# Optimization experiments

Measured on AMD Instinct MI355X. Metric: run time of the kernel, lower is better.

## Reference

```python
import jax, jax.numpy as jnp
import numpy as np

HEADS = 4
DIM_HEAD = 32


def setup_inputs() -> dict:
    key = jax.random.key(0)
    k1, k2, k3, k4, k5 = jax.random.split(key, 5)
    dim = 128
    hidden = HEADS * DIM_HEAD  # 128
    h = w = 384
    x = jax.random.normal(k1, (1, dim, h, w), dtype=jnp.float32)
    # 1x1 conv weights (eqx Conv2d layout: [out_c, in_c, 1, 1]) + biases
    w_qkv = jax.random.normal(k2, (3 * hidden, dim, 1, 1), dtype=jnp.float32) * (1.0 / np.sqrt(dim))
    b_qkv = jax.random.normal(k3, (3 * hidden,), dtype=jnp.float32) * 0.01
    w_out = jax.random.normal(k4, (dim, hidden, 1, 1), dtype=jnp.float32) * (1.0 / np.sqrt(hidden))
    b_out = jax.random.normal(k5, (dim,), dtype=jnp.float32) * 0.01
    return {"x": x, "w_qkv": w_qkv, "b_qkv": b_qkv, "w_out": w_out, "b_out": b_out}


def reference(x, w_qkv, b_qkv, w_out, b_out):
    b, c, h, w = x.shape  # b == 1 (module squeezes batch)
    xs = x[0]  # (c, h, w)
    # 1x1 conv == channel matmul
    qkv = jnp.einsum('oc,chw->ohw', w_qkv[:, :, 0, 0], xs) + b_qkv[:, None, None]
    # rearrange '(qkv heads c) h w -> qkv heads c (h w)'
    qkv = qkv.reshape(3, HEADS, DIM_HEAD, h * w)
    q, k, v = qkv[0], qkv[1], qkv[2]  # each (heads, d, n)
    k = jax.nn.softmax(k, axis=-1)
    # context: (heads, d, e) -- small per-head outer product accumulated over n
    context = jnp.einsum('hdn,hen->hde', k, v)
    out = jnp.einsum('hde,hdn->hen', context, q)  # (heads, e, n)
    out = out.reshape(HEADS * DIM_HEAD, h, w)
    y = jnp.einsum('oc,chw->ohw', w_out[:, :, 0, 0], out) + b_out[:, None, None]
    return y  # (dim, h, w) -- module returns squeezed output
```

## Files before the change

kernel.cpp:

```cpp
#include <hip/hip_runtime.h>
#include <hip/hip_bf16.h>
#include <stdint.h>


#define NPOS 147456
#define NTILES 2304
#define NB1 512

typedef __attribute__((ext_vector_type(8))) short short8;
typedef __attribute__((ext_vector_type(4))) float floatx4;

__device__ __forceinline__ uint16_t f2bf(float f) {
    uint32_t u = __float_as_uint(f);
    return (uint16_t)((u + 0x7fffu + ((u >> 16) & 1u)) >> 16);
}
__device__ __forceinline__ uint32_t pack2(float a, float b) {
#if __has_builtin(__builtin_amdgcn_cvt_pk_bf16_f32)
    auto r = __builtin_amdgcn_cvt_pk_bf16_f32(a, b);
    uint32_t u; __builtin_memcpy(&u, &r, sizeof(u));
    return u;
#else
    return (uint32_t)f2bf(a) | ((uint32_t)f2bf(b) << 16);
#endif
}

#define XS_STRIDE 68
#define PS_STRIDE 36

__global__ __launch_bounds__(256, 2) void k1_ctx(
    const float* __restrict__ x, const float* __restrict__ w_qkv,
    const float* __restrict__ b_qkv, float* __restrict__ cpart, int nb1)
{
    __shared__ uint32_t Xs[2][64 * XS_STRIDE];
    __shared__ uint32_t Ps[256 * PS_STRIDE];

    const int t = threadIdx.x;
    const int lane = t & 63;
    const int wavu = __builtin_amdgcn_readfirstlane(t >> 6);
    const int m = lane & 15, quad = lane >> 4;
    const int kvbase = wavu * 64;
    const bool is_k = (wavu < 2);
    const int c0 = wavu * 32;

    short8 wfr[4][4];
    float biasv[4];
    #pragma unroll
    for (int kt = 0; kt < 4; ++kt) {
        const int row = 128 + kvbase + kt * 16 + m;
        biasv[kt] = b_qkv[row];
        #pragma unroll
        for (int ks = 0; ks < 4; ++ks) {
            const float* p = w_qkv + row * 128 + ks * 32 + quad * 8;
            short8 w;
            #pragma unroll
            for (int j = 0; j < 8; ++j) w[j] = (short)f2bf(p[j]);
            wfr[kt][ks] = w;
        }
    }

    floatx4 acc2[4];
    #pragma unroll
    for (int i = 0; i < 4; ++i) acc2[i] = (floatx4){0.f, 0.f, 0.f, 0.f};
    float sacc[4] = {0.f, 0.f, 0.f, 0.f};

    {
        const int nofs = blockIdx.x * 64 + lane;
        float pf[32];
        #pragma unroll
        for (int i = 0; i < 32; ++i)
            pf[i] = x[(c0 + i) * NPOS + nofs];
        #pragma unroll
        for (int i = 0; i < 8; ++i) {
            uint2 w;
            w.x = pack2(pf[i * 4 + 0], pf[i * 4 + 1]);
            w.y = pack2(pf[i * 4 + 2], pf[i * 4 + 3]);
            *(uint2*)&Xs[0][lane * XS_STRIDE + (c0 + i * 4) / 2] = w;
        }
    }
    __syncthreads();

    int cur = 0;
    for (int tile = blockIdx.x; tile < NTILES; tile += nb1) {
        const int tn = tile + nb1;
        float pf[32];
        if (tn < NTILES) {
            const int nofs = tn * 64 + lane;
            #pragma unroll
            for (int i = 0; i < 32; ++i)
                pf[i] = x[(c0 + i) * NPOS + nofs];
        }
        #pragma unroll
        for (int nt = 0; nt < 4; ++nt) {
            short8 afr[4];
            #pragma unroll
            for (int ks = 0; ks < 4; ++ks)
                afr[ks] = *(const short8*)&Xs[cur][(nt * 16 + m) * XS_STRIDE + ks * 16 + quad * 4];
            floatx4 pa[4];
            #pragma unroll
            for (int kt = 0; kt < 4; ++kt) pa[kt] = (floatx4){0.f, 0.f, 0.f, 0.f};
            #pragma unroll
            for (int ks = 0; ks < 4; ++ks)
                #pragma unroll
                for (int kt = 0; kt < 4; ++kt)
                    pa[kt] = __builtin_amdgcn_mfma_f32_16x16x32_bf16(afr[ks], wfr[kt][ks], pa[kt], 0, 0, 0);
            #pragma unroll
            for (int kt = 0; kt < 4; ++kt) {
                float v0 = pa[kt][0] + biasv[kt];
                float v1 = pa[kt][1] + biasv[kt];
                float v2 = pa[kt][2] + biasv[kt];
                float v3 = pa[kt][3] + biasv[kt];
                if (is_k) {
                    v0 = __expf(v0); v1 = __expf(v1);
                    v2 = __expf(v2); v3 = __expf(v3);
                    sacc[kt] += (v0 + v1) + (v2 + v3);
                }
                uint2 w;
                w.x = pack2(v0, v1);
                w.y = pack2(v2, v3);
                const int kvrow = kvbase + kt * 16 + m;
                *(uint2*)&Ps[kvrow * PS_STRIDE + nt * 8 + quad * 2] = w;
            }
        }
        __syncthreads();
        #pragma unroll
        for (int ks = 0; ks < 2; ++ks) {
            short8 ea[2], vb[2];
            #pragma unroll
            for (int dt = 0; dt < 2; ++dt)
                ea[dt] = *(const short8*)&Ps[(wavu * 32 + dt * 16 + m) * PS_STRIDE + ks * 16 + quad * 4];
            #pragma unroll
            for (int et = 0; et < 2; ++et)
                vb[et] = *(const short8*)&Ps[(128 + wavu * 32 + et * 16 + m) * PS_STRIDE + ks * 16 + quad * 4];
            #pragma unroll
            for (int dt = 0; dt < 2; ++dt)
                #pragma unroll
                for (int et = 0; et < 2; ++et)
                    acc2[dt * 2 + et] = __builtin_amdgcn_mfma_f32_16x16x32_bf16(ea[dt], vb[et], acc2[dt * 2 + et], 0, 0, 0);
        }
        if (tn < NTILES) {
            #pragma unroll
            for (int i = 0; i < 8; ++i) {
                uint2 w;
                w.x = pack2(pf[i * 4 + 0], pf[i * 4 + 1]);
                w.y = pack2(pf[i * 4 + 2], pf[i * 4 + 3]);
                *(uint2*)&Xs[cur ^ 1][lane * XS_STRIDE + (c0 + i * 4) / 2] = w;
            }
        }
        __syncthreads();
        cur ^= 1;
    }
    float* __restrict__ dst = cpart + (size_t)blockIdx.x * 4224;
    #pragma unroll
    for (int dt = 0; dt < 2; ++dt)
        #pragma unroll
        for (int et = 0; et < 2; ++et)
            #pragma unroll
            for (int r = 0; r < 4; ++r) {
                const int d = dt * 16 + quad * 4 + r, e = et * 16 + m;
                dst[wavu * 1024 + d * 32 + e] = acc2[dt * 2 + et][r];
            }
    if (is_k) {
        #pragma unroll
        for (int kt = 0; kt < 4; ++kt) {
            float s = sacc[kt];
            s += __shfl_down(s, 32, 64);
            s += __shfl_down(s, 16, 64);
            if (lane < 16) dst[4096 + kvbase + kt * 16 + lane] = s;
        }
    }
}

__global__ void k2a(const float* __restrict__ cpart, float* __restrict__ ctxP, int nb1)
{
    const int u = blockIdx.x * 256 + threadIdx.x;
    if (u >= 4224 * 8) return;
    const int j = u % 4224, p = u / 4224;
    float s = 0.f;
    for (int b = p; b < nb1; b += 8) s += cpart[(size_t)b * 4224 + j];
    ctxP[p * 4224 + j] = s;
}

__global__ __launch_bounds__(128) void k2bc(
    const float* __restrict__ ctxP, const float* __restrict__ w_out,
    const float* __restrict__ w_qkv, const float* __restrict__ b_qkv,
    const float* __restrict__ b_out, float* __restrict__ Bm, float* __restrict__ cvec)
{
    __shared__ float ctx33[128 * 33];
    __shared__ float Ss[128];
    __shared__ float Arow[128];
    __shared__ float red[128];
    const int o = blockIdx.x, t = threadIdx.x;
    for (int j = t; j < 4224; j += 128) {
        float s = 0.f;
        #pragma unroll
        for (int p = 0; p < 8; ++p) s += ctxP[p * 4224 + j];
        if (j < 4096) ctx33[(j >> 5) * 33 + (j & 31)] = s;
        else          Ss[j - 4096] = s;
    }
    __syncthreads();
    {
        const int h = t >> 5;
        float s = 0.f;
        #pragma unroll
        for (int e = 0; e < 32; ++e)
            s = fmaf(w_out[o * 128 + h * 32 + e], ctx33[t * 33 + e], s);
        Arow[t] = s / Ss[t];
    }
    __syncthreads();
    {
        float s = 0.f;
        #pragma unroll 16
        for (int hd = 0; hd < 128; ++hd)
            s = fmaf(Arow[hd], w_qkv[hd * 128 + t], s);
        Bm[o * 128 + t] = s;
    }
    red[t] = Arow[t] * b_qkv[t];
    __syncthreads();
    if (t == 0) {
        float cs = b_out[o];
        #pragma unroll 8
        for (int i = 0; i < 128; ++i) cs += red[i];
        cvec[o] = cs;
    }
}

__global__ __launch_bounds__(256) void k3(
    const float* __restrict__ x, const float* __restrict__ Bm,
    const float* __restrict__ cvec, float* __restrict__ y)
{
    __shared__ uint32_t Xs[64 * XS_STRIDE];
    const int t = threadIdx.x, lane = t & 63;
    const int wavu = __builtin_amdgcn_readfirstlane(t >> 6);
    const int m = lane & 15, quad = lane >> 4;
    const int n0 = blockIdx.x * 64;
    const int c0 = wavu * 32;

    short8 bfr[2][4];
    float cv[2];
    #pragma unroll
    for (int ot = 0; ot < 2; ++ot) {
        const int o = (wavu * 2 + ot) * 16 + m;
        cv[ot] = cvec[o];
        #pragma unroll
        for (int ks = 0; ks < 4; ++ks) {
            const float* p = Bm + o * 128 + ks * 32 + quad * 8;
            short8 w;
            #pragma unroll
            for (int j = 0; j < 8; ++j) w[j] = (short)f2bf(p[j]);
            bfr[ot][ks] = w;
        }
    }
    {
        const int nofs = n0 + lane;
        float pf[32];
        #pragma unroll
        for (int i = 0; i < 32; ++i)
            pf[i] = x[(c0 + i) * NPOS + nofs];
        #pragma unroll
        for (int i = 0; i < 8; ++i) {
            uint2 w;
            w.x = pack2(pf[i * 4 + 0], pf[i * 4 + 1]);
            w.y = pack2(pf[i * 4 + 2], pf[i * 4 + 3]);
            *(uint2*)&Xs[lane * XS_STRIDE + (c0 + i * 4) / 2] = w;
        }
    }
    __syncthreads();
    floatx4 acc[2][4];
    #pragma unroll
    for (int ot = 0; ot < 2; ++ot)
        #pragma unroll
        for (int nt = 0; nt < 4; ++nt) acc[ot][nt] = (floatx4){0.f, 0.f, 0.f, 0.f};
    #pragma unroll
    for (int nt = 0; nt < 4; ++nt) {
        short8 afr[4];
        #pragma unroll
        for (int ks = 0; ks < 4; ++ks)
            afr[ks] = *(const short8*)&Xs[(nt * 16 + m) * XS_STRIDE + ks * 16 + quad * 4];
        #pragma unroll
        for (int ks = 0; ks < 4; ++ks)
            #pragma unroll
            for (int ot = 0; ot < 2; ++ot)
                acc[ot][nt] = __builtin_amdgcn_mfma_f32_16x16x32_bf16(afr[ks], bfr[ot][ks], acc[ot][nt], 0, 0, 0);
    }
    #pragma unroll
    for (int ot = 0; ot < 2; ++ot) {
        const int o = (wavu * 2 + ot) * 16 + m;
        #pragma unroll
        for (int nt = 0; nt < 4; ++nt) {
            floatx4 v = acc[ot][nt];
            v.x += cv[ot]; v.y += cv[ot]; v.z += cv[ot]; v.w += cv[ot];
            *(floatx4*)(y + (size_t)o * NPOS + n0 + nt * 16 + quad * 4) = v;
        }
    }
}

extern "C" void kernel_launch(void* const* d_in, const int* in_sizes, int n_in,
                              void* d_out, int out_size, void* d_ws, size_t ws_size,
                              hipStream_t stream)
{
    const float* x     = (const float*)d_in[0];
    const float* w_qkv = (const float*)d_in[1];
    const float* b_qkv = (const float*)d_in[2];
    const float* w_out = (const float*)d_in[3];
    const float* b_out = (const float*)d_in[4];
    float* y = (float*)d_out;

    const size_t tail = (size_t)(8 * 4224 + 16384 + 128) * 4;
    int nb1 = NB1;
    if (ws_size < tail + (size_t)nb1 * 16896) {
        long cap = ((long)ws_size - (long)tail) / 16896;
        nb1 = (int)cap;
        if (nb1 < 1) nb1 = 1;
        if (nb1 > NB1) nb1 = NB1;
    }
    char* wsb = (char*)d_ws;
    float* cpart = (float*)wsb;
    float* ctxP  = (float*)(wsb + (size_t)nb1 * 16896);
    float* Bm    = ctxP + 8 * 4224;
    float* cvec  = Bm + 16384;

    hipLaunchKernelGGL(k1_ctx, dim3(nb1), dim3(256), 0, stream, x, w_qkv, b_qkv, cpart, nb1);
    hipLaunchKernelGGL(k2a, dim3(132), dim3(256), 0, stream, cpart, ctxP, nb1);
    hipLaunchKernelGGL(k2bc, dim3(128), dim3(128), 0, stream, ctxP, w_out, w_qkv, b_qkv, b_out, Bm, cvec);
    hipLaunchKernelGGL(k3, dim3(NTILES), dim3(256), 0, stream, x, Bm, cvec, y);
}
```

Baseline: 206.2 us.

## Give each wave its own head's K/V, deepen prefetch, pre-pack Bm to bf16

In the context kernel, each wave now computes both K and V projections for its own head and writes them to a private LDS slice. This removes the cross-wave barrier between the projection and the context MFMA stages. The loop is unrolled by two with two register prefetch buffers, so global loads of x run two tiles ahead, at the cost of more registers. The combined output matrix is written as packed bf16 by k2bc, so k3 loads ready MFMA fragments instead of converting floats, and k3 issues its x loads before the weight loads.

Result: no change. 203.8 us (-1.2%).

```diff
diff --git a/kernel.cpp b/kernel.cpp
--- a/kernel.cpp
+++ b/kernel.cpp
@@ -27,6 +27,72 @@
 #define XS_STRIDE 68
 #define PS_STRIDE 36
 
+__device__ __forceinline__ void k1_load(const float* __restrict__ xb, float* pf) {
+    #pragma unroll
+    for (int i = 0; i < 32; ++i) pf[i] = xb[(size_t)i * NPOS];
+}
+__device__ __forceinline__ void k1_store(uint32_t* Xsbuf, const float* pf, int lane, int c0) {
+    #pragma unroll
+    for (int i = 0; i < 8; ++i) {
+        uint2 w;
+        w.x = pack2(pf[i * 4 + 0], pf[i * 4 + 1]);
+        w.y = pack2(pf[i * 4 + 2], pf[i * 4 + 3]);
+        *(uint2*)&Xsbuf[lane * XS_STRIDE + (c0 + i * 4) / 2] = w;
+    }
+}
+__device__ __forceinline__ void k1_tile(
+    const uint32_t* __restrict__ Xsbuf, uint32_t* __restrict__ Psw,
+    const short8 (&wfr)[4][4], const float (&biasv)[4],
+    floatx4 (&acc2)[4], float (&sacc)[2], int m, int quad)
+{
+    #pragma unroll
+    for (int nt = 0; nt < 4; ++nt) {
+        short8 afr[4];
+        #pragma unroll
+        for (int ks = 0; ks < 4; ++ks)
+            afr[ks] = *(const short8*)&Xsbuf[(nt * 16 + m) * XS_STRIDE + ks * 16 + quad * 4];
+        floatx4 pa[4];
+        #pragma unroll
+        for (int kt = 0; kt < 4; ++kt) pa[kt] = (floatx4){0.f, 0.f, 0.f, 0.f};
+        #pragma unroll
+        for (int ks = 0; ks < 4; ++ks)
+            #pragma unroll
+            for (int kt = 0; kt < 4; ++kt)
+                pa[kt] = __builtin_amdgcn_mfma_f32_16x16x32_bf16(afr[ks], wfr[kt][ks], pa[kt], 0, 0, 0);
+        #pragma unroll
+        for (int kt = 0; kt < 4; ++kt) {
+            float v0 = pa[kt][0] + biasv[kt];
+            float v1 = pa[kt][1] + biasv[kt];
+            float v2 = pa[kt][2] + biasv[kt];
+            float v3 = pa[kt][3] + biasv[kt];
+            if (kt < 2) {
+                v0 = __expf(v0); v1 = __expf(v1);
+                v2 = __expf(v2); v3 = __expf(v3);
+                sacc[kt] += (v0 + v1) + (v2 + v3);
+            }
+            uint2 w;
+            w.x = pack2(v0, v1);
+            w.y = pack2(v2, v3);
+            *(uint2*)&Psw[(kt * 16 + m) * PS_STRIDE + nt * 8 + quad * 2] = w;
+        }
+    }
+    #pragma unroll
+    for (int ks = 0; ks < 2; ++ks) {
+        short8 ea[2], vb[2];
+        #pragma unroll
+        for (int dt = 0; dt < 2; ++dt)
+            ea[dt] = *(const short8*)&Psw[(dt * 16 + m) * PS_STRIDE + ks * 16 + quad * 4];
+        #pragma unroll
+        for (int et = 0; et < 2; ++et)
+            vb[et] = *(const short8*)&Psw[(32 + et * 16 + m) * PS_STRIDE + ks * 16 + quad * 4];
+        #pragma unroll
+        for (int dt = 0; dt < 2; ++dt)
+            #pragma unroll
+            for (int et = 0; et < 2; ++et)
+                acc2[dt * 2 + et] = __builtin_amdgcn_mfma_f32_16x16x32_bf16(ea[dt], vb[et], acc2[dt * 2 + et], 0, 0, 0);
+    }
+}
+
 __global__ __launch_bounds__(256, 2) void k1_ctx(
     const float* __restrict__ x, const float* __restrict__ w_qkv,
     const float* __restrict__ b_qkv, float* __restrict__ cpart, int nb1)
@@ -38,15 +104,15 @@
     const int lane = t & 63;
     const int wavu = __builtin_amdgcn_readfirstlane(t >> 6);
     const int m = lane & 15, quad = lane >> 4;
-    const int kvbase = wavu * 64;
-    const bool is_k = (wavu < 2);
     const int c0 = wavu * 32;
+    uint32_t* const Psw = &Ps[wavu * 64 * PS_STRIDE];
 
     short8 wfr[4][4];
     float biasv[4];
     #pragma unroll
     for (int kt = 0; kt < 4; ++kt) {
-        const int row = 128 + kvbase + kt * 16 + m;
+        const int row = (kt < 2 ? 128 + wavu * 32 + kt * 16
+                                : 256 + wavu * 32 + (kt - 2) * 16) + m;
         biasv[kt] = b_qkv[row];
         #pragma unroll
         for (int ks = 0; ks < 4; ++ks) {
@@ -61,94 +127,30 @@
     floatx4 acc2[4];
     #pragma unroll
     for (int i = 0; i < 4; ++i) acc2[i] = (floatx4){0.f, 0.f, 0.f, 0.f};
-    float sacc[4] = {0.f, 0.f, 0.f, 0.f};
-
-    {
-        const int nofs = blockIdx.x * 64 + lane;
-        float pf[32];
-        #pragma unroll
-        for (int i = 0; i < 32; ++i)
-            pf[i] = x[(c0 + i) * NPOS + nofs];
-        #pragma unroll
-        for (int i = 0; i < 8; ++i) {
-            uint2 w;
-            w.x = pack2(pf[i * 4 + 0], pf[i * 4 + 1]);
-            w.y = pack2(pf[i * 4 + 2], pf[i * 4 + 3]);
-            *(uint2*)&Xs[0][lane * XS_STRIDE + (c0 + i * 4) / 2] = w;
+    float sacc[2] = {0.f, 0.f};
+
+    const float* xw = x + (size_t)c0 * NPOS + lane;
+    float pfA[32], pfB[32];
+
+    k1_load(xw + blockIdx.x * 64, pfA);
+    if (blockIdx.x + nb1 < NTILES) k1_load(xw + (blockIdx.x + nb1) * 64, pfB);
+    k1_store(Xs[0], pfA, lane, c0);
+    __syncthreads();
+
+    for (int tile = blockIdx.x; tile < NTILES; tile += 2 * nb1) {
+        const int t1 = tile + nb1, t2 = tile + 2 * nb1, t3 = tile + 3 * nb1;
+        if (t2 < NTILES) k1_load(xw + t2 * 64, pfA);
+        k1_tile(Xs[0], Psw, wfr, biasv, acc2, sacc, m, quad);
+        if (t1 < NTILES) k1_store(Xs[1], pfB, lane, c0);
+        __syncthreads();
+        if (t1 < NTILES) {
+            if (t3 < NTILES) k1_load(xw + t3 * 64, pfB);
+            k1_tile(Xs[1], Psw, wfr, biasv, acc2, sacc, m, quad);
+            if (t2 < NTILES) k1_store(Xs[0], pfA, lane, c0);
+            __syncthreads();
         }
     }
-    __syncthreads();
-
-    int cur = 0;
-    for (int tile = blockIdx.x; tile < NTILES; tile += nb1) {
-        const int tn = tile + nb1;
-        float pf[32];
-        if (tn < NTILES) {
-            const int nofs = tn * 64 + lane;
-            #pragma unroll
-            for (int i = 0; i < 32; ++i)
-                pf[i] = x[(c0 + i) * NPOS + nofs];
-        }
-        #pragma unroll
-        for (int nt = 0; nt < 4; ++nt) {
-            short8 afr[4];
-            #pragma unroll
-            for (int ks = 0; ks < 4; ++ks)
-                afr[ks] = *(const short8*)&Xs[cur][(nt * 16 + m) * XS_STRIDE + ks * 16 + quad * 4];
-            floatx4 pa[4];
-            #pragma unroll
-            for (int kt = 0; kt < 4; ++kt) pa[kt] = (floatx4){0.f, 0.f, 0.f, 0.f};
-            #pragma unroll
-            for (int ks = 0; ks < 4; ++ks)
-                #pragma unroll
-                for (int kt = 0; kt < 4; ++kt)
-                    pa[kt] = __builtin_amdgcn_mfma_f32_16x16x32_bf16(afr[ks], wfr[kt][ks], pa[kt], 0, 0, 0);
-            #pragma unroll
-            for (int kt = 0; kt < 4; ++kt) {
-                float v0 = pa[kt][0] + biasv[kt];
-                float v1 = pa[kt][1] + biasv[kt];
-                float v2 = pa[kt][2] + biasv[kt];
-                float v3 = pa[kt][3] + biasv[kt];
-                if (is_k) {
-                    v0 = __expf(v0); v1 = __expf(v1);
-                    v2 = __expf(v2); v3 = __expf(v3);
-                    sacc[kt] += (v0 + v1) + (v2 + v3);
-                }
-                uint2 w;
-                w.x = pack2(v0, v1);
-                w.y = pack2(v2, v3);
-                const int kvrow = kvbase + kt * 16 + m;
-                *(uint2*)&Ps[kvrow * PS_STRIDE + nt * 8 + quad * 2] = w;
-            }
-        }
-        __syncthreads();
-        #pragma unroll
-        for (int ks = 0; ks < 2; ++ks) {
-            short8 ea[2], vb[2];
-            #pragma unroll
-            for (int dt = 0; dt < 2; ++dt)
-                ea[dt] = *(const short8*)&Ps[(wavu * 32 + dt * 16 + m) * PS_STRIDE + ks * 16 + quad * 4];
-            #pragma unroll
-            for (int et = 0; et < 2; ++et)
-                vb[et] = *(const short8*)&Ps[(128 + wavu * 32 + et * 16 + m) * PS_STRIDE + ks * 16 + quad * 4];
-            #pragma unroll
-            for (int dt = 0; dt < 2; ++dt)
-                #pragma unroll
-                for (int et = 0; et < 2; ++et)
-                    acc2[dt * 2 + et] = __builtin_amdgcn_mfma_f32_16x16x32_bf16(ea[dt], vb[et], acc2[dt * 2 + et], 0, 0, 0);
-        }
-        if (tn < NTILES) {
-            #pragma unroll
-            for (int i = 0; i < 8; ++i) {
-                uint2 w;
-                w.x = pack2(pf[i * 4 + 0], pf[i * 4 + 1]);
-                w.y = pack2(pf[i * 4 + 2], pf[i * 4 + 3]);
-                *(uint2*)&Xs[cur ^ 1][lane * XS_STRIDE + (c0 + i * 4) / 2] = w;
-            }
-        }
-        __syncthreads();
-        cur ^= 1;
-    }
+
     float* __restrict__ dst = cpart + (size_t)blockIdx.x * 4224;
     #pragma unroll
     for (int dt = 0; dt < 2; ++dt)
@@ -159,14 +161,12 @@
                 const int d = dt * 16 + quad * 4 + r, e = et * 16 + m;
                 dst[wavu * 1024 + d * 32 + e] = acc2[dt * 2 + et][r];
             }
-    if (is_k) {
-        #pragma unroll
-        for (int kt = 0; kt < 4; ++kt) {
-            float s = sacc[kt];
-            s += __shfl_down(s, 32, 64);
-            s += __shfl_down(s, 16, 64);
-            if (lane < 16) dst[4096 + kvbase + kt * 16 + lane] = s;
-        }
+    #pragma unroll
+    for (int kt = 0; kt < 2; ++kt) {
+        float s = sacc[kt];
+        s += __shfl_down(s, 32, 64);
+        s += __shfl_down(s, 16, 64);
+        if (lane < 16) dst[4096 + wavu * 32 + kt * 16 + lane] = s;
     }
 }
 
@@ -183,11 +183,12 @@
 __global__ __launch_bounds__(128) void k2bc(
     const float* __restrict__ ctxP, const float* __restrict__ w_out,
     const float* __restrict__ w_qkv, const float* __restrict__ b_qkv,
-    const float* __restrict__ b_out, float* __restrict__ Bm, float* __restrict__ cvec)
+    const float* __restrict__ b_out, uint32_t* __restrict__ Bmb, float* __restrict__ cvec)
 {
     __shared__ float ctx33[128 * 33];
     __shared__ float Ss[128];
     __shared__ float Arow[128];
+    __shared__ float row[128];
     __shared__ float red[128];
     const int o = blockIdx.x, t = threadIdx.x;
     for (int j = t; j < 4224; j += 128) {
@@ -212,10 +213,11 @@
         #pragma unroll 16
         for (int hd = 0; hd < 128; ++hd)
             s = fmaf(Arow[hd], w_qkv[hd * 128 + t], s);
-        Bm[o * 128 + t] = s;
+        row[t] = s;
     }
     red[t] = Arow[t] * b_qkv[t];
     __syncthreads();
+    if (t < 64) Bmb[o * 64 + t] = pack2(row[2 * t], row[2 * t + 1]);
     if (t == 0) {
         float cs = b_out[o];
         #pragma unroll 8
@@ -225,7 +227,7 @@
 }
 
 __global__ __launch_bounds__(256) void k3(
-    const float* __restrict__ x, const float* __restrict__ Bm,
+    const float* __restrict__ x, const uint32_t* __restrict__ Bmb,
     const float* __restrict__ cvec, float* __restrict__ y)
 {
     __shared__ uint32_t Xs[64 * XS_STRIDE];
@@ -235,6 +237,9 @@
     const int n0 = blockIdx.x * 64;
     const int c0 = wavu * 32;
 
+    float pf[32];
+    k1_load(x + (size_t)c0 * NPOS + n0 + lane, pf);
+
     short8 bfr[2][4];
     float cv[2];
     #pragma unroll
@@ -242,29 +247,12 @@
         const int o = (wavu * 2 + ot) * 16 + m;
         cv[ot] = cvec[o];
         #pragma unroll
-        for (int ks = 0; ks < 4; ++ks) {
-            const float* p = Bm + o * 128 + ks * 32 + quad * 8;
-            short8 w;
-            #pragma unroll
-            for (int j = 0; j < 8; ++j) w[j] = (short)f2bf(p[j]);
-            bfr[ot][ks] = w;
-        }
-    }
-    {
-        const int nofs = n0 + lane;
-        float pf[32];
-        #pragma unroll
-        for (int i = 0; i < 32; ++i)
-            pf[i] = x[(c0 + i) * NPOS + nofs];
-        #pragma unroll
-        for (int i = 0; i < 8; ++i) {
-            uint2 w;
-            w.x = pack2(pf[i * 4 + 0], pf[i * 4 + 1]);
-            w.y = pack2(pf[i * 4 + 2], pf[i * 4 + 3]);
-            *(uint2*)&Xs[lane * XS_STRIDE + (c0 + i * 4) / 2] = w;
-        }
-    }
-    __syncthreads();
+        for (int ks = 0; ks < 4; ++ks)
+            bfr[ot][ks] = *(const short8*)&Bmb[o * 64 + ks * 16 + quad * 4];
+    }
+    k1_store(Xs, pf, lane, c0);
+    __syncthreads();
+
     floatx4 acc[2][4];
     #pragma unroll
     for (int ot = 0; ot < 2; ++ot)
@@ -305,7 +293,7 @@
     const float* b_out = (const float*)d_in[4];
     float* y = (float*)d_out;
 
-    const size_t tail = (size_t)(8 * 4224 + 16384 + 128) * 4;
+    const size_t tail = (size_t)(8 * 4224 + 8192 + 128) * 4;
     int nb1 = NB1;
     if (ws_size < tail + (size_t)nb1 * 16896) {
         long cap = ((long)ws_size - (long)tail) / 16896;
@@ -314,13 +302,13 @@
         if (nb1 > NB1) nb1 = NB1;
     }
     char* wsb = (char*)d_ws;
-    float* cpart = (float*)wsb;
-    float* ctxP  = (float*)(wsb + (size_t)nb1 * 16896);
-    float* Bm    = ctxP + 8 * 4224;
-    float* cvec  = Bm + 16384;
+    float* cpart   = (float*)wsb;
+    float* ctxP    = (float*)(wsb + (size_t)nb1 * 16896);
+    uint32_t* Bmb  = (uint32_t*)(ctxP + 8 * 4224);
+    float* cvec    = (float*)(Bmb + 8192);
 
     hipLaunchKernelGGL(k1_ctx, dim3(nb1), dim3(256), 0, stream, x, w_qkv, b_qkv, cpart, nb1);
     hipLaunchKernelGGL(k2a, dim3(132), dim3(256), 0, stream, cpart, ctxP, nb1);
-    hipLaunchKernelGGL(k2bc, dim3(128), dim3(128), 0, stream, ctxP, w_out, w_qkv, b_qkv, b_out, Bm, cvec);
-    hipLaunchKernelGGL(k3, dim3(NTILES), dim3(256), 0, stream, x, Bm, cvec, y);
-}
+    hipLaunchKernelGGL(k2bc, dim3(128), dim3(128), 0, stream, ctxP, w_out, w_qkv, b_qkv, b_out, Bmb, cvec);
+    hipLaunchKernelGGL(k3, dim3(NTILES), dim3(256), 0, stream, x, Bmb, cvec, y);
+}
```
